# Optimization experiments

Hardware: AMD Instinct MI355X
Metric: run time of the kernel (lower is better)

## Reference

```python
import jax, jax.numpy as jnp
import numpy as np

B, T, C, H = 2, 2048, 1024, 16
D = C // H
EPS = 1e-5
ROPE_BASE = 10000.0


def _rope_tables(t, d, base=ROPE_BASE):
    half = d // 2
    inv_freq = 1.0 / (base ** (jnp.arange(half, dtype=jnp.float32) / half))
    freqs = jnp.arange(t, dtype=jnp.float32)[:, None] * inv_freq[None, :]  # [T, D/2]
    emb = jnp.concatenate([freqs, freqs], axis=-1)  # [T, D]
    return jnp.cos(emb), jnp.sin(emb)


def _rotate_half(x):
    a, b = jnp.split(x, 2, axis=-1)
    return jnp.concatenate([-b, a], axis=-1)


def setup_inputs() -> dict:
    key = jax.random.key(0)
    k0, k1, k2 = jax.random.split(key, 3)
    s = 0.02  # typical init scale
    return {
        "x": jax.random.normal(k0, (B, T, C), jnp.float32),
        "attention_mask": jnp.ones((B, T), jnp.int32),
        "w_qkv": jax.random.normal(k1, (3 * C, C), jnp.float32) * s,
        "b_qkv": jnp.zeros((3 * C,), jnp.float32),
        "w_o": jax.random.normal(k2, (C, C), jnp.float32) * s,
        "b_o": jnp.zeros((C,), jnp.float32),
        "rms_w": jnp.ones((C,), jnp.float32),
    }


def reference(x, attention_mask, w_qkv, b_qkv, w_o, b_o, rms_w):
    b, t, c = x.shape
    h = H
    d = c // h
    # RMSNorm
    xn = x * jax.lax.rsqrt(jnp.mean(x * x, axis=-1, keepdims=True) + EPS) * rms_w
    # fused QKV projection -> [B, T, 3, H, D]
    qkv = (jnp.einsum('btc,oc->bto', xn, w_qkv) + b_qkv).reshape(b, t, 3, h, d)
    q, k, v = qkv[:, :, 0], qkv[:, :, 1], qkv[:, :, 2]
    # RoPE (position_ids = arange(T))
    cos, sin = _rope_tables(t, d)
    cos = cos[None, :, None, :]  # [1, T, 1, D]
    sin = sin[None, :, None, :]
    q = q * cos + _rotate_half(q) * sin
    k = k * cos + _rotate_half(k) * sin
    # causal attention (flash_attn_func semantics: scale 1/sqrt(d), causal)
    scores = jnp.einsum('bqhd,bkhd->bhqk', q, k) / jnp.sqrt(jnp.float32(d))
    causal = jnp.tril(jnp.ones((t, t), dtype=bool))
    scores = jnp.where(causal[None, None], scores, jnp.float32(-1e30))
    attn = jax.nn.softmax(scores, axis=-1)
    out = jnp.einsum('bhqk,bkhd->bqhd', attn, v).reshape(b, t, c)
    return jnp.einsum('btc,oc->bto', out, w_o) + b_o
```

## Files before the change

kernel.cpp:

```cpp
#include <hip/hip_runtime.h>
#include <math.h>

constexpr int Bb = 2;
constexpr int Tt = 2048;
constexpr int Cc = 1024;
constexpr int Hh = 16;
constexpr int M_ROWS = Bb * Tt;
constexpr float EPSV = 1e-5f;

typedef __attribute__((ext_vector_type(4))) float f32x4;
typedef __attribute__((ext_vector_type(8))) __bf16 bf16x8;
using u16 = unsigned short;

union Frag8 {
    u16 u[8];
    unsigned int ui[4];
    uint4 v;
    bf16x8 b;
};

__device__ __forceinline__ u16 f2bf(float f) {
    union { float f; unsigned int u; } c;
    c.f = f;
    unsigned int r = (c.u + 0x7fffu + ((c.u >> 16) & 1u)) >> 16;
    return (u16)r;
}
__device__ __forceinline__ float bf2f(u16 u) {
    union { unsigned int i; float f; } c;
    c.i = ((unsigned int)u) << 16;
    return c.f;
}

__device__ __forceinline__ void gload_lds16(const void* g, void* l) {
    __builtin_amdgcn_global_load_lds(
        (__attribute__((address_space(1))) void*)const_cast<void*>(g),
        (__attribute__((address_space(3))) void*)l, 16, 0, 0);
}

__global__ __launch_bounds__(256) void prep_k(const float* __restrict__ w_qkv,
                                              u16* __restrict__ wqkv_bf,
                                              const float* __restrict__ w_o,
                                              u16* __restrict__ wo_bf,
                                              float* __restrict__ cosT,
                                              float* __restrict__ sinT) {
    int blk = blockIdx.x;
    if (blk < 3072) {
        int i = (blk * 256 + threadIdx.x) * 4;
        float4 v = *(const float4*)&w_qkv[i];
        ushort4 o;
        o.x = f2bf(v.x); o.y = f2bf(v.y); o.z = f2bf(v.z); o.w = f2bf(v.w);
        *(ushort4*)&wqkv_bf[i] = o;
    } else if (blk < 4096) {
        int i = ((blk - 3072) * 256 + threadIdx.x) * 4;
        float4 v = *(const float4*)&w_o[i];
        ushort4 o;
        o.x = f2bf(v.x); o.y = f2bf(v.y); o.z = f2bf(v.z); o.w = f2bf(v.w);
        *(ushort4*)&wo_bf[i] = o;
    } else {
        int lin = (blk - 4096) * 256 + threadIdx.x;
        int tt = lin >> 5, j = lin & 31;
        float inv = exp2f(-(float)j * (log2f(10000.0f) / 32.0f));
        float a = (float)tt * inv;
        cosT[lin] = cosf(a);
        sinT[lin] = sinf(a);
    }
}

__global__ __launch_bounds__(256) void rmsnorm_k(const float* __restrict__ x,
                                                 const float* __restrict__ w,
                                                 u16* __restrict__ xn) {
    int row = blockIdx.x;
    int tid = threadIdx.x;
    const float* xr = x + (size_t)row * Cc;
    float4 v = *(const float4*)&xr[tid * 4];
    float ss = v.x * v.x + v.y * v.y + v.z * v.z + v.w * v.w;
    #pragma unroll
    for (int off = 32; off > 0; off >>= 1) ss += __shfl_down(ss, off);
    __shared__ float ws_[4];
    if ((tid & 63) == 0) ws_[tid >> 6] = ss;
    __syncthreads();
    float tot = ws_[0] + ws_[1] + ws_[2] + ws_[3];
    float r = rsqrtf(tot * (1.0f / (float)Cc) + EPSV);
    float4 wv = *(const float4*)&w[tid * 4];
    ushort4 o;
    o.x = f2bf(v.x * r * wv.x);
    o.y = f2bf(v.y * r * wv.y);
    o.z = f2bf(v.z * r * wv.z);
    o.w = f2bf(v.w * r * wv.w);
    *(ushort4*)&xn[(size_t)row * Cc + tid * 4] = o;
}

template<bool BF16OUT>
__global__ __launch_bounds__(256) void gemm_mfma_k(const u16* __restrict__ A,
                                                   const u16* __restrict__ W,
                                                   const float* __restrict__ bias,
                                                   void* __restrict__ Ov,
                                                   int M, int N, int K) {
    __shared__ __align__(16) u16 As[128 * 64];
    __shared__ __align__(16) u16 Bs[128 * 64];

    const int tid = threadIdx.x;
    const int w = tid >> 6;
    const int l = tid & 63;
    const int wr = w >> 1;
    const int wc = w & 1;
    const int q = l & 15;
    const int g = l >> 4;

    const int m0 = blockIdx.y * 128;
    const int n0 = blockIdx.x * 128;

    const int srow_in = l >> 3;
    const int p_chunk = l & 7;

    f32x4 acc[4][4];
    #pragma unroll
    for (int i = 0; i < 4; ++i)
        #pragma unroll
        for (int j = 0; j < 4; ++j)
            acc[i][j] = (f32x4){0.f, 0.f, 0.f, 0.f};

    const int nkt = K >> 6;
    for (int kt = 0; kt < nkt; ++kt) {
        const int k0 = kt << 6;
        __syncthreads();
        #pragma unroll
        for (int s = 0; s < 4; ++s) {
            int blk = s * 4 + w;
            int r = blk * 8 + srow_in;
            int c = p_chunk ^ (r & 7);
            gload_lds16(A + (size_t)(m0 + r) * K + k0 + c * 8, &As[blk * 512]);
            gload_lds16(W + (size_t)(n0 + r) * K + k0 + c * 8, &Bs[blk * 512]);
        }
        __syncthreads();

        #pragma unroll
        for (int kk = 0; kk < 2; ++kk) {
            Frag8 af[4], bf[4];
            const int ca = kk * 4 + g;
            #pragma unroll
            for (int i = 0; i < 4; ++i) {
                int ra = wr * 64 + i * 16 + q;
                af[i] = *(const Frag8*)&As[ra * 64 + ((ca ^ (ra & 7)) * 8)];
                int rb = wc * 64 + i * 16 + q;
                bf[i] = *(const Frag8*)&Bs[rb * 64 + ((ca ^ (rb & 7)) * 8)];
            }
            #pragma unroll
            for (int i = 0; i < 4; ++i)
                #pragma unroll
                for (int j = 0; j < 4; ++j)
                    acc[i][j] = __builtin_amdgcn_mfma_f32_16x16x32_bf16(
                        af[i].b, bf[j].b, acc[i][j], 0, 0, 0);
        }
    }

    #pragma unroll
    for (int i = 0; i < 4; ++i) {
        int row = m0 + wr * 64 + i * 16 + g * 4;
        #pragma unroll
        for (int j = 0; j < 4; ++j) {
            int col = n0 + wc * 64 + j * 16 + q;
            float bb = bias[col];
            #pragma unroll
            for (int r2 = 0; r2 < 4; ++r2) {
                float val = acc[i][j][r2] + bb;
                if (BF16OUT)
                    ((u16*)Ov)[(size_t)(row + r2) * N + col] = f2bf(val);
                else
                    ((float*)Ov)[(size_t)(row + r2) * N + col] = val;
            }
        }
    }
}

__global__ __launch_bounds__(256) void rope_pack_k(const u16* __restrict__ qkv,
                                                   const float* __restrict__ cosT,
                                                   const float* __restrict__ sinT,
                                                   u16* __restrict__ Qb,
                                                   u16* __restrict__ Kb,
                                                   u16* __restrict__ Vt) {
    const int t0 = blockIdx.x * 64;
    const int h = blockIdx.y, b = blockIdx.z;
    const int t = threadIdx.x;
    const int bh = b * Hh + h;
    __shared__ u16 Vs[64 * 64];
    constexpr float QSC = 0.125f * 1.44269504089f;

    {
        int row = t >> 2, d16 = (t & 3) * 16;
        const u16* vp = qkv + (size_t)(b * Tt + t0 + row) * 3072 + 2048 + h * 64 + d16;
        *(uint4*)&Vs[row * 64 + d16]     = *(const uint4*)vp;
        *(uint4*)&Vs[row * 64 + d16 + 8] = *(const uint4*)(vp + 8);
    }

    {
        int row = t >> 2, d0 = (t & 3) * 8;
        size_t rb = (size_t)(b * Tt + t0 + row) * 3072 + h * 64;
        const u16* qp = qkv + rb;
        const u16* kp = qkv + rb + 1024;
        Frag8 qlo, qhi, klo, khi;
        qlo.v = *(const uint4*)&qp[d0];
        qhi.v = *(const uint4*)&qp[d0 + 32];
        klo.v = *(const uint4*)&kp[d0];
        khi.v = *(const uint4*)&kp[d0 + 32];
        const float* cp = &cosT[(t0 + row) * 32 + d0];
        const float* sp = &sinT[(t0 + row) * 32 + d0];
        float4 c0 = *(const float4*)cp, c1 = *(const float4*)(cp + 4);
        float4 s0 = *(const float4*)sp, s1 = *(const float4*)(sp + 4);
        float cc[8] = {c0.x, c0.y, c0.z, c0.w, c1.x, c1.y, c1.z, c1.w};
        float ss[8] = {s0.x, s0.y, s0.z, s0.w, s1.x, s1.y, s1.z, s1.w};
        Frag8 oql, oqh, okl, okh;
        #pragma unroll
        for (int i = 0; i < 8; ++i) {
            float ql = bf2f(qlo.u[i]), qh = bf2f(qhi.u[i]);
            float kl = bf2f(klo.u[i]), kh = bf2f(khi.u[i]);
            oql.u[i] = f2bf((ql * cc[i] - qh * ss[i]) * QSC);
            oqh.u[i] = f2bf((qh * cc[i] + ql * ss[i]) * QSC);
            okl.u[i] = f2bf(kl * cc[i] - kh * ss[i]);
            okh.u[i] = f2bf(kh * cc[i] + kl * ss[i]);
        }
        u16* qd = Qb + ((size_t)bh * Tt + t0 + row) * 64;
        u16* kd = Kb + ((size_t)bh * Tt + t0 + row) * 64;
        *(uint4*)&qd[d0]      = oql.v;
        *(uint4*)&qd[d0 + 32] = oqh.v;
        *(uint4*)&kd[d0]      = okl.v;
        *(uint4*)&kd[d0 + 32] = okh.v;
    }
    __syncthreads();

    {
        int d = t >> 2, kq = (t & 3) * 16;
        Frag8 a, b2;
        #pragma unroll
        for (int j = 0; j < 16; ++j) {
            int slot = kq + j;
            int key = ((slot >> 5) * 2 + ((slot >> 2) & 1)) * 16
                    + ((slot >> 3) & 3) * 4 + (slot & 3);
            u16 vv = Vs[key * 64 + d];
            if (j < 8) a.u[j] = vv; else b2.u[j - 8] = vv;
        }
        u16* vd = Vt + ((size_t)bh * 64 + d) * Tt + t0 + kq;
        *(uint4*)&vd[0] = a.v;
        *(uint4*)&vd[8] = b2.v;
    }
}

__global__ __launch_bounds__(256) void attn_mfma_k(const u16* __restrict__ Qb,
                                                   const u16* __restrict__ Kb,
                                                   const u16* __restrict__ Vt,
                                                   u16* __restrict__ out) {
    const int i = blockIdx.x;
    const int p = i >> 5;
    const int bh = i & 31;
    const int cH = 31 - p, cL = p;
    const int b = bh >> 4, h = bh & 15;

    const int t = threadIdx.x;
    const int w = t >> 6;
    const int l = t & 63;
    const int q15 = l & 15;
    const int g2 = l >> 4;

    __shared__ __align__(16) u16 Ks[2][64 * 64];
    __shared__ __align__(16) u16 VTs[2][64 * 64];

    Frag8 qf[2][2];
    #pragma unroll
    for (int s = 0; s < 2; ++s) {
        int qrow = (s ? cL : cH) * 64 + w * 16 + q15;
        const u16* qp = Qb + ((size_t)bh * Tt + qrow) * 64;
        qf[s][0] = *(const Frag8*)&qp[g2 * 8];
        qf[s][1] = *(const Frag8*)&qp[32 + g2 * 8];
    }

    Frag8 ones;
    #pragma unroll
    for (int e = 0; e < 8; ++e) ones.u[e] = 0x3F80;

    f32x4 acco[2][4];
    #pragma unroll
    for (int s = 0; s < 2; ++s)
        #pragma unroll
        for (int dg = 0; dg < 4; ++dg) acco[s][dg] = (f32x4){0.f, 0.f, 0.f, 0.f};
    f32x4 acc_l[2] = {(f32x4){0.f, 0.f, 0.f, 0.f}, (f32x4){0.f, 0.f, 0.f, 0.f}};

    const int srow = l >> 3;
    const int cph = l & 7;
    const int xsw = cph ^ srow;
    const u16* Kbase = Kb + (size_t)bh * Tt * 64;
    const u16* Vbase = Vt + (size_t)bh * 64 * Tt;

    #pragma unroll
    for (int iss = 0; iss < 2; ++iss) {
        int rr = w * 16 + iss * 8 + srow;
        gload_lds16(Kbase + (size_t)rr * 64 + xsw * 8, &Ks[0][(w * 16 + iss * 8) * 64]);
        gload_lds16(Vbase + (size_t)rr * Tt + xsw * 8, &VTs[0][(w * 16 + iss * 8) * 64]);
    }
    __syncthreads();

    int cur = 0;
    for (int j = 0; j <= cH; ++j) {
        if (j < cH) {
            #pragma unroll
            for (int iss = 0; iss < 2; ++iss) {
                int rr = w * 16 + iss * 8 + srow;
                gload_lds16(Kbase + (size_t)((j + 1) * 64 + rr) * 64 + xsw * 8,
                            &Ks[cur ^ 1][(w * 16 + iss * 8) * 64]);
                gload_lds16(Vbase + (size_t)rr * Tt + (j + 1) * 64 + xsw * 8,
                            &VTs[cur ^ 1][(w * 16 + iss * 8) * 64]);
            }
        }

        const u16* Kc = Ks[cur];
        const u16* Vc = VTs[cur];

        #pragma unroll
        for (int s = 0; s < 2; ++s) {
            if (s == 1 && j > cL) continue;
            const int cc = s ? cL : cH;

            f32x4 sacc[4];
            __builtin_amdgcn_s_setprio(1);
            #pragma unroll
            for (int g = 0; g < 4; ++g) {
                sacc[g] = (f32x4){0.f, 0.f, 0.f, 0.f};
                int krow = g * 16 + q15;
                #pragma unroll
                for (int kk = 0; kk < 2; ++kk) {
                    Frag8 kf = *(const Frag8*)&Kc[krow * 64 + (((kk * 4 + g2) ^ (krow & 7)) * 8)];
                    sacc[g] = __builtin_amdgcn_mfma_f32_16x16x32_bf16(
                        kf.b, qf[s][kk].b, sacc[g], 0, 0, 0);
                }
            }
            __builtin_amdgcn_s_setprio(0);
            if (j == cc) {
                #pragma unroll
                for (int g = 0; g < 4; ++g)
                    #pragma unroll
                    for (int r = 0; r < 4; ++r)
                        if (g * 16 + g2 * 4 + r > w * 16 + q15) sacc[g][r] = -1e30f;
            }

            Frag8 pa[2];
            #pragma unroll
            for (int kk = 0; kk < 2; ++kk)
                #pragma unroll
                for (int e = 0; e < 8; ++e)
                    pa[kk].b[e] = (__bf16)exp2f(sacc[2 * kk + (e >> 2)][e & 3]);

            __builtin_amdgcn_s_setprio(1);
            acc_l[s] = __builtin_amdgcn_mfma_f32_16x16x32_bf16(pa[0].b, ones.b, acc_l[s], 0, 0, 0);
            acc_l[s] = __builtin_amdgcn_mfma_f32_16x16x32_bf16(pa[1].b, ones.b, acc_l[s], 0, 0, 0);
            #pragma unroll
            for (int dg = 0; dg < 4; ++dg) {
                int vrow = dg * 16 + q15;
                #pragma unroll
                for (int kk = 0; kk < 2; ++kk) {
                    Frag8 vf = *(const Frag8*)&Vc[vrow * 64 + (((kk * 4 + g2) ^ (vrow & 7)) * 8)];
                    acco[s][dg] = __builtin_amdgcn_mfma_f32_16x16x32_bf16(
                        pa[kk].b, vf.b, acco[s][dg], 0, 0, 0);
                }
            }
            __builtin_amdgcn_s_setprio(0);
        }

        if (j < cH) __syncthreads();
        cur ^= 1;
    }

    #pragma unroll
    for (int s = 0; s < 2; ++s) {
        float lr[4];
        #pragma unroll
        for (int r = 0; r < 4; ++r) lr[r] = 1.f / acc_l[s][r];
        const int qbase = (s ? cL : cH) * 64 + w * 16;
        #pragma unroll
        for (int dg = 0; dg < 4; ++dg)
            #pragma unroll
            for (int r = 0; r < 4; ++r)
                out[((size_t)(b * Tt + qbase + g2 * 4 + r)) * Cc + h * 64 + dg * 16 + q15] =
                    f2bf(acco[s][dg][r] * lr[r]);
    }
}

extern "C" void kernel_launch(void* const* d_in, const int* in_sizes, int n_in,
                              void* d_out, int out_size, void* d_ws, size_t ws_size,
                              hipStream_t stream) {
    const float* x      = (const float*)d_in[0];
    const float* w_qkv  = (const float*)d_in[2];
    const float* b_qkv  = (const float*)d_in[3];
    const float* w_o    = (const float*)d_in[4];
    const float* b_o    = (const float*)d_in[5];
    const float* rms_w  = (const float*)d_in[6];
    float* out = (float*)d_out;

    char* ws = (char*)d_ws;
    u16*   xn_bf   = (u16*)ws;
    u16*   Kb      = (u16*)(ws + (size_t)(8 << 20));
    u16*   Vt      = (u16*)(ws + (size_t)(16 << 20));
    u16*   Qb      = (u16*)(ws + (size_t)(24 << 20));
    u16*   qkvb    = (u16*)(ws + (size_t)(32 << 20));
    u16*   wqkv_bf = (u16*)(ws + (size_t)(56 << 20));
    u16*   wo_bf   = (u16*)(ws + (size_t)(62 << 20));
    float* cosT    = (float*)(ws + (size_t)(64 << 20));
    float* sinT    = (float*)(ws + (size_t)(64 << 20) + (1 << 18));
    u16*   attn_bf = xn_bf;

    prep_k<<<dim3(4352), dim3(256), 0, stream>>>(w_qkv, wqkv_bf, w_o, wo_bf,
                                                 cosT, sinT);
    rmsnorm_k<<<dim3(M_ROWS), dim3(256), 0, stream>>>(x, rms_w, xn_bf);
    gemm_mfma_k<true><<<dim3(3 * Cc / 128, M_ROWS / 128), dim3(256), 0, stream>>>(
        xn_bf, wqkv_bf, b_qkv, qkvb, M_ROWS, 3 * Cc, Cc);
    rope_pack_k<<<dim3(Tt / 64, Hh, Bb), dim3(256), 0, stream>>>(
        qkvb, cosT, sinT, Qb, Kb, Vt);
    attn_mfma_k<<<dim3(512), dim3(256), 0, stream>>>(Qb, Kb, Vt, attn_bf);
    gemm_mfma_k<false><<<dim3(Cc / 128, M_ROWS / 128), dim3(256), 0, stream>>>(
        attn_bf, wo_bf, b_o, out, M_ROWS, Cc, Cc);
}
```

Measured before the change: 131.3 us.

## Split paired causal q-chunks across two 4-wave teams in attention block

The attention block grows from 256 to 512 threads. Each of two 4-wave teams now owns one of the paired q-chunks (high and low), where before every wave processed both chunks in sequence. The K/V tile loads are spread over 8 waves, so each wave issues one load instead of two. This halves per-wave accumulator registers and doubles waves in flight for latency hiding. The cost is that the low-chunk team sits idle at barriers once it finishes its causal range, and larger blocks may reduce blocks per CU.

```diff
diff --git a/kernel.cpp b/kernel.cpp
--- a/kernel.cpp
+++ b/kernel.cpp
@@ -245,7 +245,7 @@
     }
 }
 
-__global__ __launch_bounds__(256) void attn_mfma_k(const u16* __restrict__ Qb,
+__global__ __launch_bounds__(512) void attn_mfma_k(const u16* __restrict__ Qb,
                                                    const u16* __restrict__ Kb,
                                                    const u16* __restrict__ Vt,
                                                    u16* __restrict__ out) {
@@ -257,6 +257,8 @@
 
     const int t = threadIdx.x;
     const int w = t >> 6;
+    const int team = w >> 2;
+    const int w4 = w & 3;
     const int l = t & 63;
     const int q15 = l & 15;
     const int g2 = l >> 4;
@@ -264,60 +266,48 @@
     __shared__ __align__(16) u16 Ks[2][64 * 64];
     __shared__ __align__(16) u16 VTs[2][64 * 64];
 
-    Frag8 qf[2][2];
-    #pragma unroll
-    for (int s = 0; s < 2; ++s) {
-        int qrow = (s ? cL : cH) * 64 + w * 16 + q15;
+    const int cc = team ? cL : cH;
+
+    Frag8 qf[2];
+    {
+        int qrow = cc * 64 + w4 * 16 + q15;
         const u16* qp = Qb + ((size_t)bh * Tt + qrow) * 64;
-        qf[s][0] = *(const Frag8*)&qp[g2 * 8];
-        qf[s][1] = *(const Frag8*)&qp[32 + g2 * 8];
+        qf[0] = *(const Frag8*)&qp[g2 * 8];
+        qf[1] = *(const Frag8*)&qp[32 + g2 * 8];
     }
 
     Frag8 ones;
     #pragma unroll
     for (int e = 0; e < 8; ++e) ones.u[e] = 0x3F80;
 
-    f32x4 acco[2][4];
-    #pragma unroll
-    for (int s = 0; s < 2; ++s)
-        #pragma unroll
-        for (int dg = 0; dg < 4; ++dg) acco[s][dg] = (f32x4){0.f, 0.f, 0.f, 0.f};
-    f32x4 acc_l[2] = {(f32x4){0.f, 0.f, 0.f, 0.f}, (f32x4){0.f, 0.f, 0.f, 0.f}};
+    f32x4 acco[4];
+    #pragma unroll
+    for (int dg = 0; dg < 4; ++dg) acco[dg] = (f32x4){0.f, 0.f, 0.f, 0.f};
+    f32x4 acc_l = (f32x4){0.f, 0.f, 0.f, 0.f};
 
     const int srow = l >> 3;
     const int cph = l & 7;
     const int xsw = cph ^ srow;
+    const int rr = w * 8 + srow;
     const u16* Kbase = Kb + (size_t)bh * Tt * 64;
     const u16* Vbase = Vt + (size_t)bh * 64 * Tt;
 
-    #pragma unroll
-    for (int iss = 0; iss < 2; ++iss) {
-        int rr = w * 16 + iss * 8 + srow;
-        gload_lds16(Kbase + (size_t)rr * 64 + xsw * 8, &Ks[0][(w * 16 + iss * 8) * 64]);
-        gload_lds16(Vbase + (size_t)rr * Tt + xsw * 8, &VTs[0][(w * 16 + iss * 8) * 64]);
-    }
+    gload_lds16(Kbase + (size_t)rr * 64 + xsw * 8, &Ks[0][(w * 8) * 64]);
+    gload_lds16(Vbase + (size_t)rr * Tt + xsw * 8, &VTs[0][(w * 8) * 64]);
     __syncthreads();
 
     int cur = 0;
     for (int j = 0; j <= cH; ++j) {
         if (j < cH) {
-            #pragma unroll
-            for (int iss = 0; iss < 2; ++iss) {
-                int rr = w * 16 + iss * 8 + srow;
-                gload_lds16(Kbase + (size_t)((j + 1) * 64 + rr) * 64 + xsw * 8,
-                            &Ks[cur ^ 1][(w * 16 + iss * 8) * 64]);
-                gload_lds16(Vbase + (size_t)rr * Tt + (j + 1) * 64 + xsw * 8,
-                            &VTs[cur ^ 1][(w * 16 + iss * 8) * 64]);
-            }
-        }
-
-        const u16* Kc = Ks[cur];
-        const u16* Vc = VTs[cur];
-
-        #pragma unroll
-        for (int s = 0; s < 2; ++s) {
-            if (s == 1 && j > cL) continue;
-            const int cc = s ? cL : cH;
+            gload_lds16(Kbase + (size_t)((j + 1) * 64 + rr) * 64 + xsw * 8,
+                        &Ks[cur ^ 1][(w * 8) * 64]);
+            gload_lds16(Vbase + (size_t)rr * Tt + (j + 1) * 64 + xsw * 8,
+                        &VTs[cur ^ 1][(w * 8) * 64]);
+        }
+
+        if (!(team == 1 && j > cL)) {
+            const u16* Kc = Ks[cur];
+            const u16* Vc = VTs[cur];
 
             f32x4 sacc[4];
             __builtin_amdgcn_s_setprio(1);
@@ -329,7 +319,7 @@
                 for (int kk = 0; kk < 2; ++kk) {
                     Frag8 kf = *(const Frag8*)&Kc[krow * 64 + (((kk * 4 + g2) ^ (krow & 7)) * 8)];
                     sacc[g] = __builtin_amdgcn_mfma_f32_16x16x32_bf16(
-                        kf.b, qf[s][kk].b, sacc[g], 0, 0, 0);
+                        kf.b, qf[kk].b, sacc[g], 0, 0, 0);
                 }
             }
             __builtin_amdgcn_s_setprio(0);
@@ -338,7 +328,7 @@
                 for (int g = 0; g < 4; ++g)
                     #pragma unroll
                     for (int r = 0; r < 4; ++r)
-                        if (g * 16 + g2 * 4 + r > w * 16 + q15) sacc[g][r] = -1e30f;
+                        if (g * 16 + g2 * 4 + r > w4 * 16 + q15) sacc[g][r] = -1e30f;
             }
 
             Frag8 pa[2];
@@ -349,16 +339,16 @@
                     pa[kk].b[e] = (__bf16)exp2f(sacc[2 * kk + (e >> 2)][e & 3]);
 
             __builtin_amdgcn_s_setprio(1);
-            acc_l[s] = __builtin_amdgcn_mfma_f32_16x16x32_bf16(pa[0].b, ones.b, acc_l[s], 0, 0, 0);
-            acc_l[s] = __builtin_amdgcn_mfma_f32_16x16x32_bf16(pa[1].b, ones.b, acc_l[s], 0, 0, 0);
+            acc_l = __builtin_amdgcn_mfma_f32_16x16x32_bf16(pa[0].b, ones.b, acc_l, 0, 0, 0);
+            acc_l = __builtin_amdgcn_mfma_f32_16x16x32_bf16(pa[1].b, ones.b, acc_l, 0, 0, 0);
             #pragma unroll
             for (int dg = 0; dg < 4; ++dg) {
                 int vrow = dg * 16 + q15;
                 #pragma unroll
                 for (int kk = 0; kk < 2; ++kk) {
                     Frag8 vf = *(const Frag8*)&Vc[vrow * 64 + (((kk * 4 + g2) ^ (vrow & 7)) * 8)];
-                    acco[s][dg] = __builtin_amdgcn_mfma_f32_16x16x32_bf16(
-                        pa[kk].b, vf.b, acco[s][dg], 0, 0, 0);
+                    acco[dg] = __builtin_amdgcn_mfma_f32_16x16x32_bf16(
+                        pa[kk].b, vf.b, acco[dg], 0, 0, 0);
                 }
             }
             __builtin_amdgcn_s_setprio(0);
@@ -368,19 +358,16 @@
         cur ^= 1;
     }
 
-    #pragma unroll
-    for (int s = 0; s < 2; ++s) {
-        float lr[4];
-        #pragma unroll
-        for (int r = 0; r < 4; ++r) lr[r] = 1.f / acc_l[s][r];
-        const int qbase = (s ? cL : cH) * 64 + w * 16;
-        #pragma unroll
-        for (int dg = 0; dg < 4; ++dg)
-            #pragma unroll
-            for (int r = 0; r < 4; ++r)
-                out[((size_t)(b * Tt + qbase + g2 * 4 + r)) * Cc + h * 64 + dg * 16 + q15] =
-                    f2bf(acco[s][dg][r] * lr[r]);
-    }
+    float lr[4];
+    #pragma unroll
+    for (int r = 0; r < 4; ++r) lr[r] = 1.f / acc_l[r];
+    const int qbase = cc * 64 + w4 * 16;
+    #pragma unroll
+    for (int dg = 0; dg < 4; ++dg)
+        #pragma unroll
+        for (int r = 0; r < 4; ++r)
+            out[((size_t)(b * Tt + qbase + g2 * 4 + r)) * Cc + h * 64 + dg * 16 + q15] =
+                f2bf(acco[dg][r] * lr[r]);
 }
 
 extern "C" void kernel_launch(void* const* d_in, const int* in_sizes, int n_in,
@@ -413,7 +400,7 @@
         xn_bf, wqkv_bf, b_qkv, qkvb, M_ROWS, 3 * Cc, Cc);
     rope_pack_k<<<dim3(Tt / 64, Hh, Bb), dim3(256), 0, stream>>>(
         qkvb, cosT, sinT, Qb, Kb, Vt);
-    attn_mfma_k<<<dim3(512), dim3(256), 0, stream>>>(Qb, Kb, Vt, attn_bf);
+    attn_mfma_k<<<dim3(512), dim3(512), 0, stream>>>(Qb, Kb, Vt, attn_bf);
     gemm_mfma_k<false><<<dim3(Cc / 128, M_ROWS / 128), dim3(256), 0, stream>>>(
         attn_bf, wo_bf, b_o, out, M_ROWS, Cc, Cc);
 }
```

Measured after the change: 127.1 us. 1.03x faster.
